# Kernel tuning notes

Measured on AMD Instinct MI355X. Metric: run time of the kernel, lower is better.

## Reference

```python
import jax, jax.numpy as jnp
import numpy as np

B, L, H, HD, FD = 1, 1024, 32, 64, 64
HID = H * HD
EPS = 1e-12


def setup_inputs() -> dict:
    key = jax.random.key(0)
    ks = jax.random.split(key, 7)
    s = 1.0 / np.sqrt(HID)
    return {
        "hidden_states": jax.random.normal(ks[0], (B, L, HID), dtype=jnp.float32),
        "Wq": jax.random.normal(ks[1], (HID, HID), dtype=jnp.float32) * s,
        "Wk": jax.random.normal(ks[2], (HID, HID), dtype=jnp.float32) * s,
        "Wv": jax.random.normal(ks[3], (HID, HID), dtype=jnp.float32) * s,
        "Wo": jax.random.normal(ks[4], (HID, HID), dtype=jnp.float32) * s,
        "Wfq": jax.random.normal(ks[5], (H, HD, FD), dtype=jnp.float32) * (1.0 / np.sqrt(HD)),
        "Wfk": jax.random.normal(ks[6], (H, HD, FD), dtype=jnp.float32) * (1.0 / np.sqrt(HD)),
    }


def _heads(x):
    # [b, l, hid] -> [b, h, l, hd]
    b, l, _ = x.shape
    return x.reshape(b, l, H, HD).transpose(0, 2, 1, 3)


def _feature_map(x, Wf):
    # per-head learned kernel + softmax over feature dim (hedgehog-style)
    z = jnp.einsum('bhld,hdf->bhlf', x, Wf)
    return jax.nn.softmax(z, axis=-1)


def _linear_attention(q, k, v, eps=EPS):
    # causal_dot_product: cumsum of outer-product KV state (fp32)
    qf, kf, vf = q.astype(jnp.float32), k.astype(jnp.float32), v.astype(jnp.float32)
    kv = jnp.cumsum(jnp.einsum('bhlf,bhld->bhlfd', kf, vf), axis=2)  # [b,h,l,f,d]
    y = jnp.einsum('bhlf,bhlfd->bhld', qf, kv)
    # fp32_attention=False branch: normalizer computed on cumsum(k)
    k_cum = jnp.cumsum(kf, axis=2).astype(q.dtype)
    denom = jnp.einsum('bhld,bhld->bhl', q, k_cum) + eps
    return y.astype(q.dtype) / denom[..., None]


def reference(hidden_states, Wq, Wk, Wv, Wo, Wfq, Wfk):
    b, l, _ = hidden_states.shape
    q = _heads(hidden_states @ Wq.T)
    k = _heads(hidden_states @ Wk.T)
    v = _heads(hidden_states @ Wv.T)
    fq = _feature_map(q, Wfq)
    fk = _feature_map(k, Wfk)
    y = _linear_attention(fq, fk, v)  # [b,h,l,hd]
    y = y.transpose(0, 2, 1, 3).reshape(b, l, HID)
    return y @ Wo.T
```

## Files before the change

### kernel.cpp

```cpp
#include <hip/hip_runtime.h>
#include <math.h>

constexpr int LQ  = 1024;
constexpr int NH  = 32;
constexpr int HDM = 64;
constexpr int FDM = 64;
constexpr int HID = 2048;
constexpr int NCH = 16;
constexpr int CT  = 64;
#define EPSV 1e-12f

typedef __bf16 bf16x8 __attribute__((ext_vector_type(8)));
typedef float  f32x4  __attribute__((ext_vector_type(4)));

__device__ __forceinline__ unsigned short f2b_raw(float x) {
    union { float f; unsigned int u; } v; v.f = x;
    unsigned int r = v.u + 0x7fffu + ((v.u >> 16) & 1u);
    return (unsigned short)(r >> 16);
}
__device__ __forceinline__ float b2f(ushort u) {
    union { unsigned int i; float f; } v; v.i = ((unsigned int)u) << 16; return v.f;
}

#define ASYNC16(ldsp, gp) __builtin_amdgcn_global_load_lds( \
    (const __attribute__((address_space(1))) void*)(gp),    \
    (__attribute__((address_space(3))) void*)(ldsp), 16, 0, 0)

template <int TM, int TN, bool BF16OUT>
__device__ __forceinline__ void gemm_core(const ushort* __restrict__ A,
                                          const ushort* __restrict__ B,
                                          void* __restrict__ Cv,
                                          int M, int N, int K) {
    constexpr int FI = TM / 32, FJ = TN / 32;
    constexpr int AI = TM / 32, BJ = TN / 32;
    constexpr int ASZ = TM * 64, BSZ = TN * 64;
    __shared__ __align__(16) ushort As[2 * ASZ];
    __shared__ __align__(16) ushort Bs[2 * BSZ];

    const int t = threadIdx.x, wave = t >> 6, lane = t & 63;
    const int wr = (wave >> 1) * (TM / 2), wc = (wave & 1) * (TN / 2);
    const int bm = blockIdx.y * TM, bn = blockIdx.x * TN;

    const int grow = lane >> 3;
    const int gsw  = ((lane & 7) ^ (grow & 7)) << 3;
    const int arow0 = wave * (TM / 4), brow0 = wave * (TN / 4);
    const ushort* gA = A + (size_t)(bm + arow0 + grow) * K + gsw;
    const ushort* gB = B + (size_t)(bn + brow0 + grow) * K + gsw;

    const int fr = lane & 15, q = lane >> 4;

    f32x4 acc[FI][FJ] = {};
    const int NIT = K >> 6;

    {
        ushort* ab = As + arow0 * 64;
        ushort* bb = Bs + brow0 * 64;
#pragma unroll
        for (int i = 0; i < AI; ++i) ASYNC16(ab + i * 512, gA + (size_t)i * 8 * K);
#pragma unroll
        for (int j = 0; j < BJ; ++j) ASYNC16(bb + j * 512, gB + (size_t)j * 8 * K);
    }
    __syncthreads();

    for (int it = 0; it < NIT; ++it) {
        const int p = it & 1;
        if (it + 1 < NIT) {
            const int ko = (it + 1) << 6;
            ushort* ab = As + (p ^ 1) * ASZ + arow0 * 64;
            ushort* bb = Bs + (p ^ 1) * BSZ + brow0 * 64;
#pragma unroll
            for (int i = 0; i < AI; ++i) ASYNC16(ab + i * 512, gA + ko + (size_t)i * 8 * K);
#pragma unroll
            for (int j = 0; j < BJ; ++j) ASYNC16(bb + j * 512, gB + ko + (size_t)j * 8 * K);
        }
        const ushort* ap = As + p * ASZ;
        const ushort* bp = Bs + p * BSZ;
        bf16x8 af[2][FI], bg[2][FJ];
#pragma unroll
        for (int ks = 0; ks < 2; ++ks) {
#pragma unroll
            for (int i = 0; i < FI; ++i) {
                const int row = wr + i * 16 + fr;
                af[ks][i] = *(const bf16x8*)&ap[row * 64 + (((q + ks * 4) ^ (row & 7)) << 3)];
            }
#pragma unroll
            for (int j = 0; j < FJ; ++j) {
                const int row = wc + j * 16 + fr;
                bg[ks][j] = *(const bf16x8*)&bp[row * 64 + (((q + ks * 4) ^ (row & 7)) << 3)];
            }
        }
#pragma unroll
        for (int ks = 0; ks < 2; ++ks)
#pragma unroll
            for (int i = 0; i < FI; ++i)
#pragma unroll
                for (int j = 0; j < FJ; ++j)
                    acc[i][j] = __builtin_amdgcn_mfma_f32_16x16x32_bf16(af[ks][i], bg[ks][j], acc[i][j], 0, 0, 0);
        if (it + 1 < NIT) __syncthreads();
    }

    const int er = q * 4, ec = lane & 15;
#pragma unroll
    for (int i = 0; i < FI; ++i)
#pragma unroll
        for (int j = 0; j < FJ; ++j) {
            const size_t base = (size_t)(bm + wr + i * 16 + er) * N + bn + wc + j * 16 + ec;
            if constexpr (BF16OUT) {
                ushort* C = (ushort*)Cv;
#pragma unroll
                for (int r = 0; r < 4; ++r) C[base + (size_t)r * N] = f2b_raw(acc[i][j][r]);
            } else {
                float* C = (float*)Cv;
#pragma unroll
                for (int r = 0; r < 4; ++r) C[base + (size_t)r * N] = acc[i][j][r];
            }
        }
}

__global__ __launch_bounds__(256) void gemm_one(const ushort* __restrict__ A,
                                                const ushort* __restrict__ B,
                                                float* __restrict__ C) {
    gemm_core<64, 64, false>(A, B, C, LQ, HID, HID);
}

__global__ __launch_bounds__(256) void gemm_qkv_fm(
    const ushort* __restrict__ hsb,
    const ushort* __restrict__ wqb, const ushort* __restrict__ wkb,
    const ushort* __restrict__ wvb,
    const ushort* __restrict__ WfqT, const ushort* __restrict__ WfkT,
    ushort* __restrict__ fqB, ushort* __restrict__ fkB,
    ushort* __restrict__ VTb) {
    constexpr int TM = 64, TN = 128;
    constexpr int ASZ = TM * 64, BSZ = TN * 64;
    __shared__ __align__(16) ushort lds[2 * ASZ + 2 * BSZ];
    ushort* As = lds;
    ushort* Bs = lds + 2 * ASZ;

    const int z = blockIdx.z;
    const ushort* Bmat = (z == 0) ? wqb : (z == 1) ? wkb : wvb;

    const int t = threadIdx.x, wave = t >> 6, lane = t & 63;
    const int wr = (wave >> 1) * 32, wc = (wave & 1) * 64;
    const int bx = blockIdx.x, c = blockIdx.y;
    const int bm = c * TM, bn = bx * TN, l0 = c * CT;

    const int grow = lane >> 3;
    const int gsw  = ((lane & 7) ^ (grow & 7)) << 3;
    const int arow0 = wave * 16, brow0 = wave * 32;
    const ushort* gA = hsb  + (size_t)(bm + arow0 + grow) * HID + gsw;
    const ushort* gB = Bmat + (size_t)(bn + brow0 + grow) * HID + gsw;

    const int fr = lane & 15, q = lane >> 4, ec = lane & 15;

    f32x4 acc[2][4] = {};
    const int NIT = HID >> 6;

    {
        ushort* ab = As + arow0 * 64;
        ushort* bb = Bs + brow0 * 64;
#pragma unroll
        for (int i = 0; i < 2; ++i) ASYNC16(ab + i * 512, gA + (size_t)i * 8 * HID);
#pragma unroll
        for (int j = 0; j < 4; ++j) ASYNC16(bb + j * 512, gB + (size_t)j * 8 * HID);
    }
    __syncthreads();

    for (int it = 0; it < NIT; ++it) {
        const int p = it & 1;
        if (it + 1 < NIT) {
            const int ko = (it + 1) << 6;
            ushort* ab = As + (p ^ 1) * ASZ + arow0 * 64;
            ushort* bb = Bs + (p ^ 1) * BSZ + brow0 * 64;
#pragma unroll
            for (int i = 0; i < 2; ++i) ASYNC16(ab + i * 512, gA + ko + (size_t)i * 8 * HID);
#pragma unroll
            for (int j = 0; j < 4; ++j) ASYNC16(bb + j * 512, gB + ko + (size_t)j * 8 * HID);
        }
        const ushort* ap = As + p * ASZ;
        const ushort* bp = Bs + p * BSZ;
        bf16x8 af[2][2], bg[2][4];
#pragma unroll
        for (int ks = 0; ks < 2; ++ks) {
#pragma unroll
            for (int i = 0; i < 2; ++i) {
                const int row = wr + i * 16 + fr;
                af[ks][i] = *(const bf16x8*)&ap[row * 64 + (((q + ks * 4) ^ (row & 7)) << 3)];
            }
#pragma unroll
            for (int j = 0; j < 4; ++j) {
                const int row = wc + j * 16 + fr;
                bg[ks][j] = *(const bf16x8*)&bp[row * 64 + (((q + ks * 4) ^ (row & 7)) << 3)];
            }
        }
#pragma unroll
        for (int ks = 0; ks < 2; ++ks)
#pragma unroll
            for (int i = 0; i < 2; ++i)
#pragma unroll
                for (int j = 0; j < 4; ++j)
                    acc[i][j] = __builtin_amdgcn_mfma_f32_16x16x32_bf16(af[ks][i], bg[ks][j], acc[i][j], 0, 0, 0);
        if (it + 1 < NIT) __syncthreads();
    }

    if (z == 2) {
#pragma unroll
        for (int i = 0; i < 2; ++i)
#pragma unroll
            for (int j = 0; j < 4; ++j) {
                const int col = wc + j * 16 + ec;
                const int hh = col >> 6, d = col & 63;
                const int lb = wr + i * 16 + q * 4;
                const size_t base = (((size_t)(2 * bx + hh) * NCH + c) * 64 + d) * 64 + lb;
                ushort4 o = make_ushort4(f2b_raw(acc[i][j][0]), f2b_raw(acc[i][j][1]),
                                         f2b_raw(acc[i][j][2]), f2b_raw(acc[i][j][3]));
                *(ushort4*)&VTb[base] = o;
            }
        return;
    }

    __syncthreads();
    ushort* Qt  = lds;
    ushort* Wfs = lds + 8704;
#pragma unroll
    for (int i = 0; i < 2; ++i)
#pragma unroll
        for (int j = 0; j < 4; ++j)
#pragma unroll
            for (int r = 0; r < 4; ++r)
                Qt[(wr + i * 16 + q * 4 + r) * 136 + wc + j * 16 + ec] = f2b_raw(acc[i][j][r]);
    {
        const ushort* WT = ((z == 0) ? WfqT : WfkT) + (size_t)(2 * bx) * 4096;
#pragma unroll
        for (int it = 0; it < 4; ++it) {
            const int e = it * 2048 + t * 8;
            const int hh = e >> 12, f = (e >> 6) & 63, dc = e & 63;
            uint4 wv4 = *(const uint4*)&WT[e];
            *(uint4*)&Wfs[hh * 4608 + f * 72 + dc] = wv4;
        }
    }
    __syncthreads();

    const int hh = wave & 1, R0 = (wave >> 1) * 32;
    f32x4 z2[2][4] = {};
#pragma unroll
    for (int ks = 0; ks < 2; ++ks) {
        bf16x8 a[2];
#pragma unroll
        for (int i = 0; i < 2; ++i)
            a[i] = *(const bf16x8*)&Qt[(R0 + i * 16 + fr) * 136 + hh * 64 + ks * 32 + q * 8];
#pragma unroll
        for (int j = 0; j < 4; ++j) {
            bf16x8 b = *(const bf16x8*)&Wfs[hh * 4608 + (j * 16 + fr) * 72 + ks * 32 + q * 8];
#pragma unroll
            for (int i = 0; i < 2; ++i)
                z2[i][j] = __builtin_amdgcn_mfma_f32_16x16x32_bf16(a[i], b, z2[i][j], 0, 0, 0);
        }
    }

    ushort* outp = (z == 0) ? fqB : fkB;
    const int hgl = 2 * bx + hh;
#pragma unroll
    for (int i = 0; i < 2; ++i)
#pragma unroll
        for (int r = 0; r < 4; ++r) {
            float m = z2[i][0][r];
#pragma unroll
            for (int j = 1; j < 4; ++j) m = fmaxf(m, z2[i][j][r]);
            m = fmaxf(m, __shfl_xor(m, 1)); m = fmaxf(m, __shfl_xor(m, 2));
            m = fmaxf(m, __shfl_xor(m, 4)); m = fmaxf(m, __shfl_xor(m, 8));
            float e4[4], s = 0.f;
#pragma unroll
            for (int j = 0; j < 4; ++j) { e4[j] = __expf(z2[i][j][r] - m); s += e4[j]; }
            s += __shfl_xor(s, 1); s += __shfl_xor(s, 2);
            s += __shfl_xor(s, 4); s += __shfl_xor(s, 8);
            const float inv = 1.0f / s;
            const int l = R0 + i * 16 + q * 4 + r;
            ushort* op = outp + ((size_t)hgl * LQ + l0 + l) * FDM;
#pragma unroll
            for (int j = 0; j < 4; ++j) op[j * 16 + ec] = f2b_raw(e4[j] * inv);
        }
}

struct ConvArgs {
    const float* src[5]; ushort* dst[5]; int n[5];
    const float* Wfq; const float* Wfk; ushort* WfqT; ushort* WfkT;
};
__global__ __launch_bounds__(256) void conv_all(ConvArgs p) {
    const int y = blockIdx.y, t = threadIdx.x;
    if (y < 5) {
        const int i = (blockIdx.x * 256 + t) * 4;
        if (i >= p.n[y]) return;
        float4 v = *(const float4*)&p.src[y][i];
        ushort4 o = make_ushort4(f2b_raw(v.x), f2b_raw(v.y), f2b_raw(v.z), f2b_raw(v.w));
        *(ushort4*)&p.dst[y][i] = o;
        return;
    }
    if (blockIdx.x >= NH) return;
    const int h = blockIdx.x;
    const float* src = ((y == 6) ? p.Wfk : p.Wfq) + (size_t)h * 4096;
    ushort* dst = ((y == 6) ? p.WfkT : p.WfqT) + (size_t)h * 4096;
    __shared__ float tile[64][65];
    for (int it = 0; it < 16; ++it) {
        int e = it * 256 + t; int d = e >> 6, f = e & 63;
        tile[d][f] = src[e];
    }
    __syncthreads();
    for (int it = 0; it < 16; ++it) {
        int e = it * 256 + t; int f = e >> 6, d = e & 63;
        dst[e] = f2b_raw(tile[d][f]);
    }
}

__global__ __launch_bounds__(256) void chunk_state(
    const ushort* __restrict__ fkB, const ushort* __restrict__ VTb,
    float* __restrict__ Sraw, float* __restrict__ Ks) {
    __shared__ __align__(16) ushort Vs[64 * 72];
    __shared__ __align__(16) ushort Fs[64 * 72];
    const int c = blockIdx.x, h = blockIdx.y;
    const int t = threadIdx.x, lane = t & 63, w = t >> 6;
    const int l0 = c * CT;
    const int fr = lane & 15, q = lane >> 4, ec = lane & 15;
    const size_t cb = ((size_t)h * NCH + c) * 4096;

    for (int it = 0; it < 2; ++it) {
        const int e = (it * 256 + t) * 8;
        const int row = e >> 6, col = e & 63;
        *(uint4*)&Vs[row * 72 + col] = *(const uint4*)&VTb[cb + e];
        uint4 fv = *(const uint4*)&fkB[((size_t)h * LQ + l0) * FDM + e];
        const ushort* pf = (const ushort*)&fv;
#pragma unroll
        for (int i2 = 0; i2 < 8; ++i2) Fs[(col + i2) * 72 + row] = pf[i2];
    }
    __syncthreads();

    f32x4 acc[4] = {};
#pragma unroll
    for (int ks = 0; ks < 2; ++ks) {
        bf16x8 a = *(const bf16x8*)&Vs[(w * 16 + fr) * 72 + ks * 32 + q * 8];
#pragma unroll
        for (int j = 0; j < 4; ++j) {
            bf16x8 b = *(const bf16x8*)&Fs[(j * 16 + fr) * 72 + ks * 32 + q * 8];
            acc[j] = __builtin_amdgcn_mfma_f32_16x16x32_bf16(a, b, acc[j], 0, 0, 0);
        }
    }
    float* sp = Sraw + cb;
#pragma unroll
    for (int j = 0; j < 4; ++j)
#pragma unroll
        for (int r = 0; r < 4; ++r)
            sp[(w * 16 + q * 4 + r) * 64 + j * 16 + ec] = acc[j][r];
    if (t < 64) {
        float s = 0.f;
#pragma unroll 8
        for (int l = 0; l < 64; ++l) s += b2f(Fs[t * 72 + l]);
        Ks[((size_t)h * NCH + c) * FDM + t] = s;
    }
}

__global__ __launch_bounds__(256) void prefix2(const float* __restrict__ Sraw,
                                               ushort* __restrict__ SpreB,
                                               const float* __restrict__ Ks,
                                               float* __restrict__ Kpre) {
    const int h = blockIdx.x, eb = blockIdx.y, t = threadIdx.x;
    const int e0 = eb * 512 + t * 2;
    float r0 = 0.f, r1 = 0.f;
    const size_t hb = (size_t)h * NCH * 4096;
    for (int c2 = 0; c2 < NCH; ++c2) {
        const size_t base = hb + (size_t)c2 * 4096 + e0;
        float c0 = Sraw[base], c1 = Sraw[base + 1];
        ushort2 o = make_ushort2(f2b_raw(r0), f2b_raw(r1));
        *(ushort2*)&SpreB[base] = o;
        r0 += c0; r1 += c1;
    }
    if (eb == 0 && t < 64) {
        float rk = 0.f;
        for (int c2 = 0; c2 < NCH; ++c2) {
            const size_t kb2 = ((size_t)h * NCH + c2) * FDM + t;
            float cur = Ks[kb2];
            Kpre[kb2] = rk;
            rk += cur;
        }
    }
}

__global__ __launch_bounds__(256) void intra2(
    const ushort* __restrict__ fqB, const ushort* __restrict__ fkB,
    const ushort* __restrict__ VTb, const ushort* __restrict__ SpreB,
    const float* __restrict__ Kpre, ushort* __restrict__ Yb) {
    __shared__ __align__(16) ushort fqs[64 * 72];
    __shared__ __align__(16) ushort fks[64 * 72];
    __shared__ __align__(16) ushort VTs[64 * 72];
    __shared__ __align__(16) ushort Sps[64 * 72];
    __shared__ __align__(16) ushort Pms[64 * 72];
    __shared__ float den[64], kpr[64];

    const int c = blockIdx.x, h = blockIdx.y;
    const int t = threadIdx.x, lane = t & 63, wave = t >> 6;
    const int l0 = c * CT;
    const int fr = lane & 15, fo = (lane >> 4) * 8;
    const int g = lane >> 4, cc = lane & 15;

    const size_t qkbase = ((size_t)h * LQ + l0) * FDM;
    const size_t cbase  = ((size_t)h * NCH + c) * 4096;
    for (int it = 0; it < 2; ++it) {
        int e = (it * 256 + t) * 8;
        int row = e >> 6, col = e & 63;
        *(uint4*)&fqs[row * 72 + col] = *(const uint4*)&fqB[qkbase + e];
        *(uint4*)&fks[row * 72 + col] = *(const uint4*)&fkB[qkbase + e];
        *(uint4*)&VTs[row * 72 + col] = *(const uint4*)&VTb[cbase + e];
        *(uint4*)&Sps[row * 72 + col] = *(const uint4*)&SpreB[cbase + e];
    }
    if (t < 64) kpr[t] = Kpre[((size_t)h * NCH + c) * FDM + t];
    __syncthreads();

    f32x4 accP[4] = {};
#pragma unroll
    for (int kp = 0; kp < 2; ++kp) {
        bf16x8 a = *(const bf16x8*)&fqs[(wave * 16 + fr) * 72 + kp * 32 + fo];
#pragma unroll
        for (int j = 0; j < 4; ++j) {
            bf16x8 b = *(const bf16x8*)&fks[(j * 16 + fr) * 72 + kp * 32 + fo];
            accP[j] = __builtin_amdgcn_mfma_f32_16x16x32_bf16(a, b, accP[j], 0, 0, 0);
        }
    }
#pragma unroll
    for (int j = 0; j < 4; ++j)
#pragma unroll
        for (int r = 0; r < 4; ++r) {
            int l = wave * 16 + g * 4 + r, lp = j * 16 + cc;
            Pms[l * 72 + lp] = (lp <= l) ? f2b_raw(accP[j][r]) : (ushort)0;
        }
    __syncthreads();

    {
        const int srow = t >> 2, spart = t & 3;
        float s = 0.f;
#pragma unroll
        for (int i = 0; i < 16; ++i) s += b2f(Pms[srow * 72 + spart * 16 + i]);
#pragma unroll
        for (int i = 0; i < 16; ++i) s += b2f(fqs[srow * 72 + spart * 16 + i]) * kpr[spart * 16 + i];
        s += __shfl_xor(s, 1); s += __shfl_xor(s, 2);
        if (spart == 0) den[srow] = s + EPSV;
    }
    __syncthreads();

    f32x4 accY[4] = {};
#pragma unroll
    for (int kp = 0; kp < 2; ++kp) {
        bf16x8 a = *(const bf16x8*)&Pms[(wave * 16 + fr) * 72 + kp * 32 + fo];
#pragma unroll
        for (int j = 0; j < 4; ++j) {
            bf16x8 b = *(const bf16x8*)&VTs[(j * 16 + fr) * 72 + kp * 32 + fo];
            accY[j] = __builtin_amdgcn_mfma_f32_16x16x32_bf16(a, b, accY[j], 0, 0, 0);
        }
    }
#pragma unroll
    for (int kp = 0; kp < 2; ++kp) {
        bf16x8 a = *(const bf16x8*)&fqs[(wave * 16 + fr) * 72 + kp * 32 + fo];
#pragma unroll
        for (int j = 0; j < 4; ++j) {
            bf16x8 b = *(const bf16x8*)&Sps[(j * 16 + fr) * 72 + kp * 32 + fo];
            accY[j] = __builtin_amdgcn_mfma_f32_16x16x32_bf16(a, b, accY[j], 0, 0, 0);
        }
    }
#pragma unroll
    for (int r = 0; r < 4; ++r) {
        int l = wave * 16 + g * 4 + r;
        float inv = 1.0f / den[l];
        ushort* yo = Yb + (size_t)(l0 + l) * HID + h * HDM;
#pragma unroll
        for (int j = 0; j < 4; ++j)
            yo[j * 16 + cc] = f2b_raw(accY[j][r] * inv);
    }
}

extern "C" void kernel_launch(void* const* d_in, const int* in_sizes, int n_in,
                              void* d_out, int out_size, void* d_ws, size_t ws_size,
                              hipStream_t stream) {
    const float* hs  = (const float*)d_in[0];
    const float* Wq  = (const float*)d_in[1];
    const float* Wk  = (const float*)d_in[2];
    const float* Wv  = (const float*)d_in[3];
    const float* Wo  = (const float*)d_in[4];
    const float* Wfq = (const float*)d_in[5];
    const float* Wfk = (const float*)d_in[6];
    float* out = (float*)d_out;

    const size_t SZ = (size_t)LQ * HID;
    const size_t WZ = (size_t)HID * HID;

    char* w = (char*)d_ws;
    auto aus = [&](size_t n) { ushort* p = (ushort*)w; w += n * sizeof(ushort); return p; };
    auto afl = [&](size_t n) { float*  p = (float*)w;  w += n * sizeof(float);  return p; };

    ushort* hsb   = aus(SZ);
    ushort* wqb   = aus(WZ);
    ushort* wkb   = aus(WZ);
    ushort* wvb   = aus(WZ);
    ushort* wob   = aus(WZ);
    ushort* fqB   = aus(SZ);
    ushort* fkB   = aus(SZ);
    ushort* VTb   = aus(SZ);
    ushort* WfqT  = aus((size_t)NH * 4096);
    ushort* WfkT  = aus((size_t)NH * 4096);
    ushort* SpreB = aus(SZ);
    ushort* Yb    = aus(SZ);
    float*  Sraw  = afl(SZ);
    float*  Ks    = afl((size_t)NH * NCH * FDM);
    float*  Kpre  = afl((size_t)NH * NCH * FDM);

    ConvArgs ca;
    ca.src[0] = hs; ca.dst[0] = hsb; ca.n[0] = (int)SZ;
    ca.src[1] = Wq; ca.dst[1] = wqb; ca.n[1] = (int)WZ;
    ca.src[2] = Wk; ca.dst[2] = wkb; ca.n[2] = (int)WZ;
    ca.src[3] = Wv; ca.dst[3] = wvb; ca.n[3] = (int)WZ;
    ca.src[4] = Wo; ca.dst[4] = wob; ca.n[4] = (int)WZ;
    ca.Wfq = Wfq; ca.Wfk = Wfk; ca.WfqT = WfqT; ca.WfkT = WfkT;
    conv_all<<<dim3((unsigned)(WZ / 1024), 7), 256, 0, stream>>>(ca);

    gemm_qkv_fm<<<dim3(HID / 128, LQ / 64, 3), 256, 0, stream>>>(
        hsb, wqb, wkb, wvb, WfqT, WfkT, fqB, fkB, VTb);

    chunk_state<<<dim3(NCH, NH), 256, 0, stream>>>(fkB, VTb, Sraw, Ks);

    prefix2<<<dim3(NH, 8), 256, 0, stream>>>(Sraw, SpreB, Ks, Kpre);

    intra2<<<dim3(NCH, NH), 256, 0, stream>>>(fqB, fkB, VTb, SpreB, Kpre, Yb);

    gemm_one<<<dim3(HID / 64, LQ / 64), 256, 0, stream>>>(Yb, wob, out);
}
```

Measured before the change: 195.2 us.

## Fuse chunk state computation and prefix scan into one sequential scan kernel

```diff
diff --git a/kernel.cpp b/kernel.cpp
--- a/kernel.cpp
+++ b/kernel.cpp
@@ -311,74 +311,46 @@
     }
 }
 
-__global__ __launch_bounds__(256) void chunk_state(
+__global__ __launch_bounds__(256) void state_scan(
     const ushort* __restrict__ fkB, const ushort* __restrict__ VTb,
-    float* __restrict__ Sraw, float* __restrict__ Ks) {
-    __shared__ __align__(16) ushort Vs[64 * 72];
-    __shared__ __align__(16) ushort Fs[64 * 72];
-    const int c = blockIdx.x, h = blockIdx.y;
-    const int t = threadIdx.x, lane = t & 63, w = t >> 6;
-    const int l0 = c * CT;
-    const int fr = lane & 15, q = lane >> 4, ec = lane & 15;
-    const size_t cb = ((size_t)h * NCH + c) * 4096;
-
-    for (int it = 0; it < 2; ++it) {
-        const int e = (it * 256 + t) * 8;
-        const int row = e >> 6, col = e & 63;
-        *(uint4*)&Vs[row * 72 + col] = *(const uint4*)&VTb[cb + e];
-        uint4 fv = *(const uint4*)&fkB[((size_t)h * LQ + l0) * FDM + e];
-        const ushort* pf = (const ushort*)&fv;
-#pragma unroll
-        for (int i2 = 0; i2 < 8; ++i2) Fs[(col + i2) * 72 + row] = pf[i2];
-    }
-    __syncthreads();
-
-    f32x4 acc[4] = {};
-#pragma unroll
-    for (int ks = 0; ks < 2; ++ks) {
-        bf16x8 a = *(const bf16x8*)&Vs[(w * 16 + fr) * 72 + ks * 32 + q * 8];
-#pragma unroll
-        for (int j = 0; j < 4; ++j) {
-            bf16x8 b = *(const bf16x8*)&Fs[(j * 16 + fr) * 72 + ks * 32 + q * 8];
-            acc[j] = __builtin_amdgcn_mfma_f32_16x16x32_bf16(a, b, acc[j], 0, 0, 0);
-        }
-    }
-    float* sp = Sraw + cb;
-#pragma unroll
-    for (int j = 0; j < 4; ++j)
-#pragma unroll
-        for (int r = 0; r < 4; ++r)
-            sp[(w * 16 + q * 4 + r) * 64 + j * 16 + ec] = acc[j][r];
-    if (t < 64) {
-        float s = 0.f;
+    ushort* __restrict__ SpreB, float* __restrict__ Kpre) {
+    __shared__ __align__(16) ushort fks[64 * 64];
+    __shared__ __align__(16) ushort vts[8 * 64];
+    const int h = blockIdx.x, eb = blockIdx.y, t = threadIdx.x;
+    const int dr0 = eb * 8;
+    const int dloc = t >> 5, f = (t * 2) & 63;
+    float run0 = 0.f, run1 = 0.f, rk = 0.f;
+
+    for (int c = 0; c < NCH; ++c) {
+        __syncthreads();
+        {
+            const int e = t * 16;
+            const size_t fb = ((size_t)h * LQ + c * CT) * FDM;
+            *(uint4*)&fks[e]     = *(const uint4*)&fkB[fb + e];
+            *(uint4*)&fks[e + 8] = *(const uint4*)&fkB[fb + e + 8];
+            if (t < 64) {
+                const size_t vb = (((size_t)h * NCH + c) * 64 + dr0) * 64;
+                *(uint4*)&vts[t * 8] = *(const uint4*)&VTb[vb + t * 8];
+            }
+        }
+        __syncthreads();
+
+        const size_t sbase = ((size_t)h * NCH + c) * 4096 + dr0 * 64 + t * 2;
+        ushort2 pr = make_ushort2(f2b_raw(run0), f2b_raw(run1));
+        *(ushort2*)&SpreB[sbase] = pr;
+
 #pragma unroll 8
-        for (int l = 0; l < 64; ++l) s += b2f(Fs[t * 72 + l]);
-        Ks[((size_t)h * NCH + c) * FDM + t] = s;
-    }
-}
-
-__global__ __launch_bounds__(256) void prefix2(const float* __restrict__ Sraw,
-                                               ushort* __restrict__ SpreB,
-                                               const float* __restrict__ Ks,
-                                               float* __restrict__ Kpre) {
-    const int h = blockIdx.x, eb = blockIdx.y, t = threadIdx.x;
-    const int e0 = eb * 512 + t * 2;
-    float r0 = 0.f, r1 = 0.f;
-    const size_t hb = (size_t)h * NCH * 4096;
-    for (int c2 = 0; c2 < NCH; ++c2) {
-        const size_t base = hb + (size_t)c2 * 4096 + e0;
-        float c0 = Sraw[base], c1 = Sraw[base + 1];
-        ushort2 o = make_ushort2(f2b_raw(r0), f2b_raw(r1));
-        *(ushort2*)&SpreB[base] = o;
-        r0 += c0; r1 += c1;
-    }
-    if (eb == 0 && t < 64) {
-        float rk = 0.f;
-        for (int c2 = 0; c2 < NCH; ++c2) {
-            const size_t kb2 = ((size_t)h * NCH + c2) * FDM + t;
-            float cur = Ks[kb2];
-            Kpre[kb2] = rk;
-            rk += cur;
+        for (int l = 0; l < 64; ++l) {
+            const float vt = b2f(vts[dloc * 64 + l]);
+            run0 += vt * b2f(fks[l * 64 + f]);
+            run1 += vt * b2f(fks[l * 64 + f + 1]);
+        }
+        if (eb == 0 && t < 64) {
+            Kpre[((size_t)h * NCH + c) * FDM + t] = rk;
+            float s = 0.f;
+#pragma unroll 8
+            for (int l = 0; l < 64; ++l) s += b2f(fks[l * 64 + t]);
+            rk += s;
         }
     }
 }
@@ -505,8 +477,6 @@
     ushort* WfkT  = aus((size_t)NH * 4096);
     ushort* SpreB = aus(SZ);
     ushort* Yb    = aus(SZ);
-    float*  Sraw  = afl(SZ);
-    float*  Ks    = afl((size_t)NH * NCH * FDM);
     float*  Kpre  = afl((size_t)NH * NCH * FDM);
 
     ConvArgs ca;
@@ -521,9 +491,7 @@
     gemm_qkv_fm<<<dim3(HID / 128, LQ / 64, 3), 256, 0, stream>>>(
         hsb, wqb, wkb, wvb, WfqT, WfkT, fqB, fkB, VTb);
 
-    chunk_state<<<dim3(NCH, NH), 256, 0, stream>>>(fkB, VTb, Sraw, Ks);
-
-    prefix2<<<dim3(NH, 8), 256, 0, stream>>>(Sraw, SpreB, Ks, Kpre);
+    state_scan<<<dim3(NH, 8), 256, 0, stream>>>(fkB, VTb, SpreB, Kpre);
 
     intra2<<<dim3(NCH, NH), 256, 0, stream>>>(fqB, fkB, VTb, SpreB, Kpre, Yb);
 
```

Result: slower. 224.7 us (+15.1%).

## Fuse chunk-state prefix sum into intra-chunk kernel and flatten conversion grid

Applied to the files above, without the earlier changes.

```diff
diff --git a/kernel.cpp b/kernel.cpp
--- a/kernel.cpp
+++ b/kernel.cpp
@@ -282,23 +282,25 @@
 }
 
 struct ConvArgs {
-    const float* src[5]; ushort* dst[5]; int n[5];
+    const float* src[5]; ushort* dst[5];
     const float* Wfq; const float* Wfk; ushort* WfqT; ushort* WfkT;
 };
 __global__ __launch_bounds__(256) void conv_all(ConvArgs p) {
-    const int y = blockIdx.y, t = threadIdx.x;
-    if (y < 5) {
-        const int i = (blockIdx.x * 256 + t) * 4;
-        if (i >= p.n[y]) return;
-        float4 v = *(const float4*)&p.src[y][i];
+    const int b = blockIdx.x, t = threadIdx.x;
+    if (b < 18432) {
+        int g = b * 256 + t;
+        int which; int off;
+        if (g < 524288) { which = 0; off = g; }
+        else { g -= 524288; which = 1 + (g >> 20); off = g & 1048575; }
+        const size_t e = (size_t)off * 4;
+        float4 v = *(const float4*)&p.src[which][e];
         ushort4 o = make_ushort4(f2b_raw(v.x), f2b_raw(v.y), f2b_raw(v.z), f2b_raw(v.w));
-        *(ushort4*)&p.dst[y][i] = o;
+        *(ushort4*)&p.dst[which][e] = o;
         return;
     }
-    if (blockIdx.x >= NH) return;
-    const int h = blockIdx.x;
-    const float* src = ((y == 6) ? p.Wfk : p.Wfq) + (size_t)h * 4096;
-    ushort* dst = ((y == 6) ? p.WfkT : p.WfqT) + (size_t)h * 4096;
+    const int idx = b - 18432, h = idx & 31, isK = idx >> 5;
+    const float* src = (isK ? p.Wfk : p.Wfq) + (size_t)h * 4096;
+    ushort* dst = (isK ? p.WfkT : p.WfqT) + (size_t)h * 4096;
     __shared__ float tile[64][65];
     for (int it = 0; it < 16; ++it) {
         int e = it * 256 + t; int d = e >> 6, f = e & 63;
@@ -357,36 +359,10 @@
     }
 }
 
-__global__ __launch_bounds__(256) void prefix2(const float* __restrict__ Sraw,
-                                               ushort* __restrict__ SpreB,
-                                               const float* __restrict__ Ks,
-                                               float* __restrict__ Kpre) {
-    const int h = blockIdx.x, eb = blockIdx.y, t = threadIdx.x;
-    const int e0 = eb * 512 + t * 2;
-    float r0 = 0.f, r1 = 0.f;
-    const size_t hb = (size_t)h * NCH * 4096;
-    for (int c2 = 0; c2 < NCH; ++c2) {
-        const size_t base = hb + (size_t)c2 * 4096 + e0;
-        float c0 = Sraw[base], c1 = Sraw[base + 1];
-        ushort2 o = make_ushort2(f2b_raw(r0), f2b_raw(r1));
-        *(ushort2*)&SpreB[base] = o;
-        r0 += c0; r1 += c1;
-    }
-    if (eb == 0 && t < 64) {
-        float rk = 0.f;
-        for (int c2 = 0; c2 < NCH; ++c2) {
-            const size_t kb2 = ((size_t)h * NCH + c2) * FDM + t;
-            float cur = Ks[kb2];
-            Kpre[kb2] = rk;
-            rk += cur;
-        }
-    }
-}
-
 __global__ __launch_bounds__(256) void intra2(
     const ushort* __restrict__ fqB, const ushort* __restrict__ fkB,
-    const ushort* __restrict__ VTb, const ushort* __restrict__ SpreB,
-    const float* __restrict__ Kpre, ushort* __restrict__ Yb) {
+    const ushort* __restrict__ VTb, const float* __restrict__ Sraw,
+    const float* __restrict__ Ks, ushort* __restrict__ Yb) {
     __shared__ __align__(16) ushort fqs[64 * 72];
     __shared__ __align__(16) ushort fks[64 * 72];
     __shared__ __align__(16) ushort VTs[64 * 72];
@@ -408,9 +384,30 @@
         *(uint4*)&fqs[row * 72 + col] = *(const uint4*)&fqB[qkbase + e];
         *(uint4*)&fks[row * 72 + col] = *(const uint4*)&fkB[qkbase + e];
         *(uint4*)&VTs[row * 72 + col] = *(const uint4*)&VTb[cbase + e];
-        *(uint4*)&Sps[row * 72 + col] = *(const uint4*)&SpreB[cbase + e];
-    }
-    if (t < 64) kpr[t] = Kpre[((size_t)h * NCH + c) * FDM + t];
+    }
+    {
+        float pre[16] = {};
+        const size_t hb = (size_t)h * NCH * 4096;
+        for (int c2 = 0; c2 < c; ++c2) {
+            const float* sp = Sraw + hb + (size_t)c2 * 4096 + t * 16;
+#pragma unroll
+            for (int i = 0; i < 16; i += 4) {
+                float4 v = *(const float4*)&sp[i];
+                pre[i] += v.x; pre[i + 1] += v.y; pre[i + 2] += v.z; pre[i + 3] += v.w;
+            }
+        }
+        const int row = (t * 16) >> 6, col = (t * 16) & 63;
+        ushort o[16];
+#pragma unroll
+        for (int i = 0; i < 16; ++i) o[i] = f2b_raw(pre[i]);
+        *(uint4*)&Sps[row * 72 + col]     = *(uint4*)&o[0];
+        *(uint4*)&Sps[row * 72 + col + 8] = *(uint4*)&o[8];
+        if (t < 64) {
+            float rk = 0.f;
+            for (int c2 = 0; c2 < c; ++c2) rk += Ks[((size_t)h * NCH + c2) * FDM + t];
+            kpr[t] = rk;
+        }
+    }
     __syncthreads();
 
     f32x4 accP[4] = {};
@@ -503,29 +500,25 @@
     ushort* VTb   = aus(SZ);
     ushort* WfqT  = aus((size_t)NH * 4096);
     ushort* WfkT  = aus((size_t)NH * 4096);
-    ushort* SpreB = aus(SZ);
     ushort* Yb    = aus(SZ);
     float*  Sraw  = afl(SZ);
     float*  Ks    = afl((size_t)NH * NCH * FDM);
-    float*  Kpre  = afl((size_t)NH * NCH * FDM);
 
     ConvArgs ca;
-    ca.src[0] = hs; ca.dst[0] = hsb; ca.n[0] = (int)SZ;
-    ca.src[1] = Wq; ca.dst[1] = wqb; ca.n[1] = (int)WZ;
-    ca.src[2] = Wk; ca.dst[2] = wkb; ca.n[2] = (int)WZ;
-    ca.src[3] = Wv; ca.dst[3] = wvb; ca.n[3] = (int)WZ;
-    ca.src[4] = Wo; ca.dst[4] = wob; ca.n[4] = (int)WZ;
+    ca.src[0] = hs; ca.dst[0] = hsb;
+    ca.src[1] = Wq; ca.dst[1] = wqb;
+    ca.src[2] = Wk; ca.dst[2] = wkb;
+    ca.src[3] = Wv; ca.dst[3] = wvb;
+    ca.src[4] = Wo; ca.dst[4] = wob;
     ca.Wfq = Wfq; ca.Wfk = Wfk; ca.WfqT = WfqT; ca.WfkT = WfkT;
-    conv_all<<<dim3((unsigned)(WZ / 1024), 7), 256, 0, stream>>>(ca);
+    conv_all<<<18496, 256, 0, stream>>>(ca);
 
     gemm_qkv_fm<<<dim3(HID / 128, LQ / 64, 3), 256, 0, stream>>>(
         hsb, wqb, wkb, wvb, WfqT, WfkT, fqB, fkB, VTb);
 
     chunk_state<<<dim3(NCH, NH), 256, 0, stream>>>(fkB, VTb, Sraw, Ks);
 
-    prefix2<<<dim3(NH, 8), 256, 0, stream>>>(Sraw, SpreB, Ks, Kpre);
-
-    intra2<<<dim3(NCH, NH), 256, 0, stream>>>(fqB, fkB, VTb, SpreB, Kpre, Yb);
+    intra2<<<dim3(NCH, NH), 256, 0, stream>>>(fqB, fkB, VTb, Sraw, Ks, Yb);
 
     gemm_one<<<dim3(HID / 64, LQ / 64), 256, 0, stream>>>(Yb, wob, out);
 }
```

After: 201.3 us. 3.1% more time.
